# Optimization experiments

Measured on AMD Instinct MI355X. Metric: run time of the kernel, lower is better.

The kernel has to match this reference:

```python
import jax, jax.numpy as jnp
import numpy as np

B, S, H, NH = 2, 2048, 1024, 16
D = H // NH

def setup_inputs() -> dict:
    key = jax.random.key(0)
    ks = jax.random.split(key, 9)
    s = 1.0 / np.sqrt(H)
    return {
        "x": jax.random.normal(ks[0], (B, S, H), jnp.float32),
        "wq": jax.random.uniform(ks[1], (H, H), jnp.float32, -s, s),
        "bq": jax.random.uniform(ks[2], (H,), jnp.float32, -s, s),
        "wk": jax.random.uniform(ks[3], (H, H), jnp.float32, -s, s),
        "bk": jax.random.uniform(ks[4], (H,), jnp.float32, -s, s),
        "wv": jax.random.uniform(ks[5], (H, H), jnp.float32, -s, s),
        "bv": jax.random.uniform(ks[6], (H,), jnp.float32, -s, s),
        "wo": jax.random.uniform(ks[7], (H, H), jnp.float32, -s, s),
        "bo": jax.random.uniform(ks[8], (H,), jnp.float32, -s, s),
    }

def _split_heads(t):
    # [B, S, H] -> [B, NH, S, D]
    return t.reshape(B, S, NH, D).transpose(0, 2, 1, 3)

def reference(x, wq, bq, wk, bk, wv, bv, wo, bo):
    q = _split_heads(x @ wq.T + bq)
    k = _split_heads(x @ wk.T + bk)
    v = _split_heads(x @ wv.T + bv)
    scores = jnp.einsum('bhqd,bhkd->bhqk', q, k) / jnp.sqrt(jnp.float32(D))
    attn = jax.nn.softmax(scores, axis=-1)  # full [B,NH,S,S] materialized as in source
    ctx = jnp.einsum('bhqk,bhkd->bhqd', attn, v)
    concat = ctx.transpose(0, 2, 1, 3).reshape(B, S, H)
    return concat @ wo.T + bo
```

## Files before the change

kernel.cpp:

```cpp
#include <hip/hip_runtime.h>
#include <cstdint>

typedef unsigned short u16;
typedef __attribute__((ext_vector_type(8))) short short8;
typedef __attribute__((ext_vector_type(4))) float f32x4;

#if __has_builtin(__builtin_amdgcn_exp2f)
#define EXP2F(x) __builtin_amdgcn_exp2f(x)
#else
#define EXP2F(x) exp2f(x)
#endif

__device__ inline u16 f2bf(float f) {
  union { float f; unsigned u; } v; v.f = f;
  unsigned u = v.u;
  return (u16)((u + 0x7fffu + ((u >> 16) & 1u)) >> 16);
}

__device__ inline unsigned pk2bf_fast(float a, float b) {
  union { float f; unsigned u; } ua, ub; ua.f = a; ub.f = b;
  return __builtin_amdgcn_perm(ub.u + 0x8000u, ua.u + 0x8000u, 0x07060302u);
}

__device__ inline void gl2lds16(const void* g, void* l) {
  __builtin_amdgcn_global_load_lds(
      (const __attribute__((address_space(1))) unsigned int*)(unsigned long long)(uintptr_t)g,
      (__attribute__((address_space(3))) unsigned int*)(unsigned int)(uintptr_t)l,
      16, 0, 0);
}


__global__ __launch_bounds__(256) void cvt_kernel(
    const float* __restrict__ x,
    const float* __restrict__ wq, const float* __restrict__ wk,
    const float* __restrict__ wv, const float* __restrict__ wo,
    u16* __restrict__ xb, u16* __restrict__ wqb, u16* __restrict__ wkb,
    u16* __restrict__ wvb, u16* __restrict__ wob) {
  const int y = blockIdx.y;
  const int Q = 1 << 20;
  const float* src;
  u16* dst;
  if (y < 4)       { src = x + y * Q; dst = xb + y * Q; }
  else if (y == 4) { src = wq; dst = wqb; }
  else if (y == 5) { src = wk; dst = wkb; }
  else if (y == 6) { src = wv; dst = wvb; }
  else             { src = wo; dst = wob; }
  const int i = (blockIdx.x * 256 + threadIdx.x) * 8;
  float4 a = *(const float4*)(src + i);
  float4 b = *(const float4*)(src + i + 4);
  short8 o;
  o[0] = (short)f2bf(a.x); o[1] = (short)f2bf(a.y);
  o[2] = (short)f2bf(a.z); o[3] = (short)f2bf(a.w);
  o[4] = (short)f2bf(b.x); o[5] = (short)f2bf(b.y);
  o[6] = (short)f2bf(b.z); o[7] = (short)f2bf(b.w);
  const int j = (i & ~63) | (((((i >> 3) & 7) ^ ((i >> 10) & 7))) << 3);
  *(short8*)(dst + j) = o;
}

__global__ __launch_bounds__(256) void gemm_qkv(
    const u16* __restrict__ xb,
    const u16* __restrict__ wqb, const u16* __restrict__ wkb, const u16* __restrict__ wvb,
    const float* __restrict__ bq, const float* __restrict__ bk, const float* __restrict__ bv,
    u16* __restrict__ qo, u16* __restrict__ ko, u16* __restrict__ vto) {
  const int z = blockIdx.z;
  const u16* W = (z == 0) ? wqb : (z == 1) ? wkb : wvb;
  const float* bias = (z == 0) ? bq : (z == 1) ? bk : bv;

  __shared__ u16 smem[24576];
  u16* As = smem;
  u16* Bs = smem + 16384;
  const int tid = threadIdx.x, lane = tid & 63;
  const int wid = tid >> 6;
  const int l15 = lane & 15, lg = lane >> 4;
  const int m0 = blockIdx.y * 128, n0 = blockIdx.x * 64;
  const int sw = ((l15 & 7) << 3);

  f32x4 acc[2][4] = {};

#pragma unroll
  for (int i = 0; i < 4; ++i) {
    int c = i * 256 + tid;
    gl2lds16(xb + (m0 + (c >> 3)) * 1024 + (c & 7) * 8, As + c * 8);
  }
#pragma unroll
  for (int i = 0; i < 2; ++i) {
    int c = i * 256 + tid;
    gl2lds16(W + (n0 + (c >> 3)) * 1024 + (c & 7) * 8, Bs + c * 8);
  }

  for (int k0 = 0; k0 < 1024; k0 += 64) {
    const int p = (k0 >> 6) & 1;
    __syncthreads();
    if (k0 < 960) {
      u16* An = As + (1 - p) * 8192;
      u16* Bn = Bs + (1 - p) * 4096;
#pragma unroll
      for (int i = 0; i < 4; ++i) {
        int c = i * 256 + tid;
        gl2lds16(xb + (m0 + (c >> 3)) * 1024 + k0 + 64 + (c & 7) * 8, An + c * 8);
      }
#pragma unroll
      for (int i = 0; i < 2; ++i) {
        int c = i * 256 + tid;
        gl2lds16(W + (n0 + (c >> 3)) * 1024 + k0 + 64 + (c & 7) * 8, Bn + c * 8);
      }
    }
    const u16* Ap = As + p * 8192;
    const u16* Bp = Bs + p * 4096;
#pragma unroll
    for (int kk = 0; kk < 2; ++kk) {
      short8 af[2], bf[4];
#pragma unroll
      for (int mb = 0; mb < 2; ++mb)
        af[mb] = *(const short8*)(Ap + (wid * 32 + mb * 16 + l15) * 64 + ((((kk * 4 + lg) << 3)) ^ sw));
#pragma unroll
      for (int nb = 0; nb < 4; ++nb)
        bf[nb] = *(const short8*)(Bp + (nb * 16 + l15) * 64 + ((((kk * 4 + lg) << 3)) ^ sw));
#pragma unroll
      for (int mb = 0; mb < 2; ++mb)
#pragma unroll
        for (int nb = 0; nb < 4; ++nb)
          acc[mb][nb] = __builtin_amdgcn_mfma_f32_16x16x32_bf16(af[mb], bf[nb], acc[mb][nb], 0, 0, 0);
    }
  }

  if (z < 2) {
    u16* out = (z == 0) ? qo : ko;
#pragma unroll
    for (int mb = 0; mb < 2; ++mb)
#pragma unroll
      for (int nb = 0; nb < 4; ++nb)
#pragma unroll
        for (int r = 0; r < 4; ++r) {
          int m = m0 + wid * 32 + mb * 16 + lg * 4 + r;
          int n = n0 + nb * 16 + l15;
          float v = acc[mb][nb][r] + bias[n];
          int b = m >> 11, s = m & 2047, hh = n >> 6, d = n & 63;
          out[((b * 16 + hh) * 2048 + s) * 64 + d] = f2bf(v);
        }
  } else {
    __syncthreads();
    u16* wbuf = smem + (wid >> 1) * 4608;
    const int so = (wid & 1) * 2;
#pragma unroll
    for (int mb = 0; mb < 2; ++mb)
#pragma unroll
      for (int nb = 0; nb < 4; ++nb) {
        int n = n0 + nb * 16 + l15;
        float bn = bias[n];
        int dl = nb * 16 + l15;
#pragma unroll
        for (int r = 0; r < 4; ++r) {
          int sig = (lg * 4 + r) * 4 + so + mb;
          wbuf[dl * 72 + sig] = f2bf(acc[mb][nb][r] + bn);
        }
      }
    __syncthreads();
    int hh = n0 >> 6;
    int bb = m0 >> 11;
    int sbase = m0 & 2047;
#pragma unroll
    for (int i = 0; i < 4; ++i) {
      int idx = i * 256 + tid;
      int p2 = idx >> 9, rem = idx & 511;
      int dl = rem >> 3, c = rem & 7;
      short8 vv = *(const short8*)(smem + p2 * 4608 + dl * 72 + c * 8);
      int cs = c ^ (dl & 7);
      *(short8*)(vto + ((bb * 16 + hh) * 64 + dl) * 2048 + sbase + p2 * 64 + cs * 8) = vv;
    }
  }
}

__global__ __launch_bounds__(256, 2) void attn_kernel(
    const u16* __restrict__ qg, const u16* __restrict__ kg,
    const u16* __restrict__ vtg, u16* __restrict__ ctxg) {
  const int h = blockIdx.x, qt = blockIdx.y, b = blockIdx.z;
  const int bh = b * 16 + h;
  const u16* Qg = qg + (bh * 2048 + qt * 128) * 64;
  const u16* Kg = kg + bh * 2048 * 64;
  const u16* Vg = vtg + bh * 64 * 2048;

  __shared__ u16 SP[128 * 72];
  __shared__ u16 Vs[2][4096];

  const int tid = threadIdx.x, lane = tid & 63, wid = tid >> 6;
  const int l15 = lane & 15, lg = lane >> 4;
  const int row0 = wid * 32;
  const int sw = ((l15 & 7) << 3);

  short8 qf[2][2];
#pragma unroll
  for (int mb = 0; mb < 2; ++mb)
#pragma unroll
    for (int kk = 0; kk < 2; ++kk)
      qf[mb][kk] = *(const short8*)(Qg + (row0 + mb * 16 + l15) * 64 + kk * 32 + lg * 8);

  short8 ones8;
#pragma unroll
  for (int j = 0; j < 8; ++j) ones8[j] = (short)0x3F80;

  const u16* kbase = Kg + l15 * 64 + lg * 8;

  short8 kf[2][4];
#pragma unroll
  for (int kk = 0; kk < 2; ++kk)
#pragma unroll
    for (int nb = 0; nb < 4; ++nb)
      kf[kk][nb] = *(const short8*)(kbase + nb * 1024 + kk * 32);

#pragma unroll
  for (int i = 0; i < 2; ++i) {
    int c = i * 256 + tid;
    gl2lds16(Vg + (c >> 3) * 2048 + (c & 7) * 8, &Vs[0][c * 8]);
  }

  f32x4 acc[2][5] = {};
  const float cexp = 0.18033688011112042f;

  for (int kt = 0; kt < 32; ++kt) {
    const int p = kt & 1;
    __syncthreads();
    if (kt < 31) {
#pragma unroll
      for (int i = 0; i < 2; ++i) {
        int c = i * 256 + tid;
        gl2lds16(Vg + (c >> 3) * 2048 + (kt + 1) * 64 + (c & 7) * 8, &Vs[1 - p][c * 8]);
      }
    }
    const u16* Vts = &Vs[p][0];

    f32x4 sc[2][4] = {};
#pragma unroll
    for (int kk = 0; kk < 2; ++kk)
#pragma unroll
      for (int mb = 0; mb < 2; ++mb)
#pragma unroll
        for (int nb = 0; nb < 4; ++nb)
          sc[mb][nb] = __builtin_amdgcn_mfma_f32_16x16x32_bf16(qf[mb][kk], kf[kk][nb], sc[mb][nb], 0, 0, 0);

#pragma unroll
    for (int mb = 0; mb < 2; ++mb)
#pragma unroll
      for (int r = 0; r < 4; ++r) {
        float p0 = EXP2F(fmaf(sc[mb][0][r], cexp, -4.0f));
        float p1 = EXP2F(fmaf(sc[mb][1][r], cexp, -4.0f));
        float p2 = EXP2F(fmaf(sc[mb][2][r], cexp, -4.0f));
        float p3 = EXP2F(fmaf(sc[mb][3][r], cexp, -4.0f));
        uint2 u;
        u.x = pk2bf_fast(p0, p1);
        u.y = pk2bf_fast(p2, p3);
        *(uint2*)(SP + (row0 + mb * 16 + lg * 4 + r) * 72 + l15 * 4) = u;
      }

    {
      const int ktn = (kt + 1 < 32) ? kt + 1 : 0;
#pragma unroll
      for (int kk = 0; kk < 2; ++kk)
#pragma unroll
        for (int nb = 0; nb < 4; ++nb)
          kf[kk][nb] = *(const short8*)(kbase + ktn * 4096 + nb * 1024 + kk * 32);
    }

#pragma unroll
    for (int kk = 0; kk < 2; ++kk) {
      short8 pa[2], vb[4];
#pragma unroll
      for (int mb = 0; mb < 2; ++mb)
        pa[mb] = *(const short8*)(SP + (row0 + mb * 16 + l15) * 72 + kk * 32 + lg * 8);
#pragma unroll
      for (int nd = 0; nd < 4; ++nd)
        vb[nd] = *(const short8*)(Vts + (nd * 16 + l15) * 64 + ((((kk * 4 + lg) << 3)) ^ sw));
#pragma unroll
      for (int mb = 0; mb < 2; ++mb) {
#pragma unroll
        for (int nd = 0; nd < 4; ++nd)
          acc[mb][nd] = __builtin_amdgcn_mfma_f32_16x16x32_bf16(pa[mb], vb[nd], acc[mb][nd], 0, 0, 0);
        acc[mb][4] = __builtin_amdgcn_mfma_f32_16x16x32_bf16(pa[mb], ones8, acc[mb][4], 0, 0, 0);
      }
    }
  }

#pragma unroll
  for (int mb = 0; mb < 2; ++mb)
#pragma unroll
    for (int r = 0; r < 4; ++r) {
      float inv = 1.0f / acc[mb][4][r];
      int s = qt * 128 + row0 + mb * 16 + lg * 4 + r;
      int s7 = s & 7;
      u16* dst = ctxg + (b * 2048 + s) * 1024 + h * 64;
#pragma unroll
      for (int nd = 0; nd < 4; ++nd) {
        int d = nd * 16 + l15;
        int dcol = (((d >> 3) ^ s7) << 3) | (d & 7);
        dst[dcol] = f2bf(acc[mb][nd][r] * inv);
      }
    }
}

__global__ __launch_bounds__(256) void gemm_out(
    const u16* __restrict__ cb, const u16* __restrict__ wob,
    const float* __restrict__ bo, float* __restrict__ out) {
  __shared__ u16 smem[16384];
  u16* As = smem;
  u16* Bs = smem + 8192;
  const int tid = threadIdx.x, lane = tid & 63;
  const int wid = tid >> 6;
  const int l15 = lane & 15, lg = lane >> 4;
  const int m0 = blockIdx.y * 64, n0 = blockIdx.x * 64;
  const int sw = ((l15 & 7) << 3);

  f32x4 acc[4] = {};

#pragma unroll
  for (int i = 0; i < 2; ++i) {
    int c = i * 256 + tid;
    gl2lds16(cb  + (m0 + (c >> 3)) * 1024 + (c & 7) * 8, As + c * 8);
    gl2lds16(wob + (n0 + (c >> 3)) * 1024 + (c & 7) * 8, Bs + c * 8);
  }

  for (int k0 = 0; k0 < 1024; k0 += 64) {
    const int p = (k0 >> 6) & 1;
    __syncthreads();
    if (k0 < 960) {
      u16* An = As + (1 - p) * 4096;
      u16* Bn = Bs + (1 - p) * 4096;
#pragma unroll
      for (int i = 0; i < 2; ++i) {
        int c = i * 256 + tid;
        gl2lds16(cb  + (m0 + (c >> 3)) * 1024 + k0 + 64 + (c & 7) * 8, An + c * 8);
        gl2lds16(wob + (n0 + (c >> 3)) * 1024 + k0 + 64 + (c & 7) * 8, Bn + c * 8);
      }
    }
    const u16* Ap = As + p * 4096;
    const u16* Bp = Bs + p * 4096;
#pragma unroll
    for (int kk = 0; kk < 2; ++kk) {
      short8 af, bf[4];
      af = *(const short8*)(Ap + (wid * 16 + l15) * 64 + ((((kk * 4 + lg) << 3)) ^ sw));
#pragma unroll
      for (int nb = 0; nb < 4; ++nb)
        bf[nb] = *(const short8*)(Bp + (nb * 16 + l15) * 64 + ((((kk * 4 + lg) << 3)) ^ sw));
#pragma unroll
      for (int nb = 0; nb < 4; ++nb)
        acc[nb] = __builtin_amdgcn_mfma_f32_16x16x32_bf16(af, bf[nb], acc[nb], 0, 0, 0);
    }
  }

#pragma unroll
  for (int nb = 0; nb < 4; ++nb)
#pragma unroll
    for (int r = 0; r < 4; ++r) {
      int m = m0 + wid * 16 + lg * 4 + r;
      int n = n0 + nb * 16 + l15;
      out[m * 1024 + n] = acc[nb][r] + bo[n];
    }
}

extern "C" void kernel_launch(void* const* d_in, const int* in_sizes, int n_in,
                              void* d_out, int out_size, void* d_ws, size_t ws_size,
                              hipStream_t stream) {
  const float* x  = (const float*)d_in[0];
  const float* wq = (const float*)d_in[1];
  const float* bq = (const float*)d_in[2];
  const float* wk = (const float*)d_in[3];
  const float* bk = (const float*)d_in[4];
  const float* wv = (const float*)d_in[5];
  const float* bv = (const float*)d_in[6];
  const float* wo = (const float*)d_in[7];
  const float* bo = (const float*)d_in[8];

  if (ws_size < (size_t)24 * 1024 * 1024 * 2) return;
  u16* xb   = (u16*)d_ws;
  u16* wqb  = xb  + (4u << 20);
  u16* wkb  = wqb + (1u << 20);
  u16* wvb  = wkb + (1u << 20);
  u16* wob  = wvb + (1u << 20);
  u16* qb   = wob + (1u << 20);
  u16* kb   = qb  + (4u << 20);
  u16* vtb  = kb  + (4u << 20);
  u16* ctxb = vtb + (4u << 20);

  cvt_kernel<<<dim3(512, 8, 1), 256, 0, stream>>>(x, wq, wk, wv, wo, xb, wqb, wkb, wvb, wob);
  gemm_qkv<<<dim3(16, 32, 3), 256, 0, stream>>>(xb, wqb, wkb, wvb, bq, bk, bv, qb, kb, vtb);
  attn_kernel<<<dim3(16, 16, 2), 256, 0, stream>>>(qb, kb, vtb, ctxb);
  gemm_out<<<dim3(16, 64, 1), 256, 0, stream>>>(ctxb, wob, bo, (float*)d_out);
}
```

Measured before the change: 202.7 us.

## Fuse Q/K/V projections per block, prescale Q, stage K through LDS

The QKV GEMM now computes Q, K and V in one block, so each x tile loaded into LDS is reused by three weight tiles instead of being reloaded across three grid z-slices. The grid shrinks to a third, and LDS and accumulator registers per block grow. The softmax scale is folded into Q at store time, and the constant exp offset is dropped. K is written with an XOR-swizzled column layout. In attention, K is double-buffered through LDS with async copies alongside V, replacing the per-lane global register prefetch. The trade-offs are fewer blocks with higher register and LDS pressure, and a small risk of exp range issues without the offset.

```diff
diff --git a/kernel.cpp b/kernel.cpp
--- a/kernel.cpp
+++ b/kernel.cpp
@@ -57,16 +57,12 @@
   *(short8*)(dst + j) = o;
 }
 
-__global__ __launch_bounds__(256) void gemm_qkv(
+__global__ __launch_bounds__(256, 2) void gemm_qkv(
     const u16* __restrict__ xb,
     const u16* __restrict__ wqb, const u16* __restrict__ wkb, const u16* __restrict__ wvb,
     const float* __restrict__ bq, const float* __restrict__ bk, const float* __restrict__ bv,
     u16* __restrict__ qo, u16* __restrict__ ko, u16* __restrict__ vto) {
-  const int z = blockIdx.z;
-  const u16* W = (z == 0) ? wqb : (z == 1) ? wkb : wvb;
-  const float* bias = (z == 0) ? bq : (z == 1) ? bk : bv;
-
-  __shared__ u16 smem[24576];
+  __shared__ u16 smem[40960];
   u16* As = smem;
   u16* Bs = smem + 16384;
   const int tid = threadIdx.x, lane = tid & 63;
@@ -74,8 +70,9 @@
   const int l15 = lane & 15, lg = lane >> 4;
   const int m0 = blockIdx.y * 128, n0 = blockIdx.x * 64;
   const int sw = ((l15 & 7) << 3);
-
-  f32x4 acc[2][4] = {};
+  const u16* Wz[3] = {wqb, wkb, wvb};
+
+  f32x4 acc[3][2][4] = {};
 
 #pragma unroll
   for (int i = 0; i < 4; ++i) {
@@ -83,63 +80,86 @@
     gl2lds16(xb + (m0 + (c >> 3)) * 1024 + (c & 7) * 8, As + c * 8);
   }
 #pragma unroll
-  for (int i = 0; i < 2; ++i) {
-    int c = i * 256 + tid;
-    gl2lds16(W + (n0 + (c >> 3)) * 1024 + (c & 7) * 8, Bs + c * 8);
-  }
+  for (int z = 0; z < 3; ++z)
+#pragma unroll
+    for (int i = 0; i < 2; ++i) {
+      int c = i * 256 + tid;
+      gl2lds16(Wz[z] + (n0 + (c >> 3)) * 1024 + (c & 7) * 8, Bs + z * 4096 + c * 8);
+    }
 
   for (int k0 = 0; k0 < 1024; k0 += 64) {
     const int p = (k0 >> 6) & 1;
     __syncthreads();
     if (k0 < 960) {
       u16* An = As + (1 - p) * 8192;
-      u16* Bn = Bs + (1 - p) * 4096;
+      u16* Bn = Bs + (1 - p) * 12288;
 #pragma unroll
       for (int i = 0; i < 4; ++i) {
         int c = i * 256 + tid;
         gl2lds16(xb + (m0 + (c >> 3)) * 1024 + k0 + 64 + (c & 7) * 8, An + c * 8);
       }
 #pragma unroll
-      for (int i = 0; i < 2; ++i) {
-        int c = i * 256 + tid;
-        gl2lds16(W + (n0 + (c >> 3)) * 1024 + k0 + 64 + (c & 7) * 8, Bn + c * 8);
-      }
+      for (int z = 0; z < 3; ++z)
+#pragma unroll
+        for (int i = 0; i < 2; ++i) {
+          int c = i * 256 + tid;
+          gl2lds16(Wz[z] + (n0 + (c >> 3)) * 1024 + k0 + 64 + (c & 7) * 8, Bn + z * 4096 + c * 8);
+        }
     }
     const u16* Ap = As + p * 8192;
-    const u16* Bp = Bs + p * 4096;
+    const u16* Bp = Bs + p * 12288;
 #pragma unroll
     for (int kk = 0; kk < 2; ++kk) {
-      short8 af[2], bf[4];
+      short8 af[2], bf[3][4];
 #pragma unroll
       for (int mb = 0; mb < 2; ++mb)
         af[mb] = *(const short8*)(Ap + (wid * 32 + mb * 16 + l15) * 64 + ((((kk * 4 + lg) << 3)) ^ sw));
 #pragma unroll
-      for (int nb = 0; nb < 4; ++nb)
-        bf[nb] = *(const short8*)(Bp + (nb * 16 + l15) * 64 + ((((kk * 4 + lg) << 3)) ^ sw));
-#pragma unroll
-      for (int mb = 0; mb < 2; ++mb)
+      for (int z = 0; z < 3; ++z)
 #pragma unroll
         for (int nb = 0; nb < 4; ++nb)
-          acc[mb][nb] = __builtin_amdgcn_mfma_f32_16x16x32_bf16(af[mb], bf[nb], acc[mb][nb], 0, 0, 0);
-    }
-  }
-
-  if (z < 2) {
-    u16* out = (z == 0) ? qo : ko;
-#pragma unroll
-    for (int mb = 0; mb < 2; ++mb)
-#pragma unroll
-      for (int nb = 0; nb < 4; ++nb)
-#pragma unroll
-        for (int r = 0; r < 4; ++r) {
-          int m = m0 + wid * 32 + mb * 16 + lg * 4 + r;
-          int n = n0 + nb * 16 + l15;
-          float v = acc[mb][nb][r] + bias[n];
-          int b = m >> 11, s = m & 2047, hh = n >> 6, d = n & 63;
-          out[((b * 16 + hh) * 2048 + s) * 64 + d] = f2bf(v);
-        }
-  } else {
-    __syncthreads();
+          bf[z][nb] = *(const short8*)(Bp + z * 4096 + (nb * 16 + l15) * 64 + ((((kk * 4 + lg) << 3)) ^ sw));
+#pragma unroll
+      for (int z = 0; z < 3; ++z)
+#pragma unroll
+        for (int mb = 0; mb < 2; ++mb)
+#pragma unroll
+          for (int nb = 0; nb < 4; ++nb)
+            acc[z][mb][nb] = __builtin_amdgcn_mfma_f32_16x16x32_bf16(af[mb], bf[z][nb], acc[z][mb][nb], 0, 0, 0);
+    }
+  }
+
+  const float cexp = 0.18033688011112042f;
+
+#pragma unroll
+  for (int mb = 0; mb < 2; ++mb)
+#pragma unroll
+    for (int nb = 0; nb < 4; ++nb)
+#pragma unroll
+      for (int r = 0; r < 4; ++r) {
+        int m = m0 + wid * 32 + mb * 16 + lg * 4 + r;
+        int n = n0 + nb * 16 + l15;
+        float v = (acc[0][mb][nb][r] + bq[n]) * cexp;
+        int b = m >> 11, s = m & 2047, hh = n >> 6, d = n & 63;
+        qo[((b * 16 + hh) * 2048 + s) * 64 + d] = f2bf(v);
+      }
+
+#pragma unroll
+  for (int mb = 0; mb < 2; ++mb)
+#pragma unroll
+    for (int nb = 0; nb < 4; ++nb)
+#pragma unroll
+      for (int r = 0; r < 4; ++r) {
+        int m = m0 + wid * 32 + mb * 16 + lg * 4 + r;
+        int n = n0 + nb * 16 + l15;
+        float v = acc[1][mb][nb][r] + bk[n];
+        int b = m >> 11, s = m & 2047, hh = n >> 6, d = n & 63;
+        int dcol = (((d >> 3) ^ (s & 7)) << 3) | (d & 7);
+        ko[((b * 16 + hh) * 2048 + s) * 64 + dcol] = f2bf(v);
+      }
+
+  __syncthreads();
+  {
     u16* wbuf = smem + (wid >> 1) * 4608;
     const int so = (wid & 1) * 2;
 #pragma unroll
@@ -147,12 +167,12 @@
 #pragma unroll
       for (int nb = 0; nb < 4; ++nb) {
         int n = n0 + nb * 16 + l15;
-        float bn = bias[n];
+        float bn = bv[n];
         int dl = nb * 16 + l15;
 #pragma unroll
         for (int r = 0; r < 4; ++r) {
           int sig = (lg * 4 + r) * 4 + so + mb;
-          wbuf[dl * 72 + sig] = f2bf(acc[mb][nb][r] + bn);
+          wbuf[dl * 72 + sig] = f2bf(acc[2][mb][nb][r] + bn);
         }
       }
     __syncthreads();
@@ -181,7 +201,7 @@
   const u16* Vg = vtg + bh * 64 * 2048;
 
   __shared__ u16 SP[128 * 72];
-  __shared__ u16 Vs[2][4096];
+  __shared__ u16 KV[2][8192];
 
   const int tid = threadIdx.x, lane = tid & 63, wid = tid >> 6;
   const int l15 = lane & 15, lg = lane >> 4;
@@ -199,23 +219,14 @@
 #pragma unroll
   for (int j = 0; j < 8; ++j) ones8[j] = (short)0x3F80;
 
-  const u16* kbase = Kg + l15 * 64 + lg * 8;
-
-  short8 kf[2][4];
-#pragma unroll
-  for (int kk = 0; kk < 2; ++kk)
-#pragma unroll
-    for (int nb = 0; nb < 4; ++nb)
-      kf[kk][nb] = *(const short8*)(kbase + nb * 1024 + kk * 32);
-
 #pragma unroll
   for (int i = 0; i < 2; ++i) {
     int c = i * 256 + tid;
-    gl2lds16(Vg + (c >> 3) * 2048 + (c & 7) * 8, &Vs[0][c * 8]);
+    gl2lds16(Kg + c * 8, &KV[0][c * 8]);
+    gl2lds16(Vg + (c >> 3) * 2048 + (c & 7) * 8, &KV[0][4096 + c * 8]);
   }
 
   f32x4 acc[2][5] = {};
-  const float cexp = 0.18033688011112042f;
 
   for (int kt = 0; kt < 32; ++kt) {
     const int p = kt & 1;
@@ -224,42 +235,40 @@
 #pragma unroll
       for (int i = 0; i < 2; ++i) {
         int c = i * 256 + tid;
-        gl2lds16(Vg + (c >> 3) * 2048 + (kt + 1) * 64 + (c & 7) * 8, &Vs[1 - p][c * 8]);
-      }
-    }
-    const u16* Vts = &Vs[p][0];
+        gl2lds16(Kg + (kt + 1) * 4096 + c * 8, &KV[1 - p][c * 8]);
+        gl2lds16(Vg + (c >> 3) * 2048 + (kt + 1) * 64 + (c & 7) * 8, &KV[1 - p][4096 + c * 8]);
+      }
+    }
+    const u16* Ks = &KV[p][0];
+    const u16* Vts = &KV[p][4096];
 
     f32x4 sc[2][4] = {};
 #pragma unroll
-    for (int kk = 0; kk < 2; ++kk)
+    for (int kk = 0; kk < 2; ++kk) {
+      short8 bfr[4];
+#pragma unroll
+      for (int nb = 0; nb < 4; ++nb)
+        bfr[nb] = *(const short8*)(Ks + (nb * 16 + l15) * 64 + ((((kk * 4 + lg) << 3)) ^ sw));
 #pragma unroll
       for (int mb = 0; mb < 2; ++mb)
 #pragma unroll
         for (int nb = 0; nb < 4; ++nb)
-          sc[mb][nb] = __builtin_amdgcn_mfma_f32_16x16x32_bf16(qf[mb][kk], kf[kk][nb], sc[mb][nb], 0, 0, 0);
+          sc[mb][nb] = __builtin_amdgcn_mfma_f32_16x16x32_bf16(qf[mb][kk], bfr[nb], sc[mb][nb], 0, 0, 0);
+    }
 
 #pragma unroll
     for (int mb = 0; mb < 2; ++mb)
 #pragma unroll
       for (int r = 0; r < 4; ++r) {
-        float p0 = EXP2F(fmaf(sc[mb][0][r], cexp, -4.0f));
-        float p1 = EXP2F(fmaf(sc[mb][1][r], cexp, -4.0f));
-        float p2 = EXP2F(fmaf(sc[mb][2][r], cexp, -4.0f));
-        float p3 = EXP2F(fmaf(sc[mb][3][r], cexp, -4.0f));
+        float p0 = EXP2F(sc[mb][0][r]);
+        float p1 = EXP2F(sc[mb][1][r]);
+        float p2 = EXP2F(sc[mb][2][r]);
+        float p3 = EXP2F(sc[mb][3][r]);
         uint2 u;
         u.x = pk2bf_fast(p0, p1);
         u.y = pk2bf_fast(p2, p3);
         *(uint2*)(SP + (row0 + mb * 16 + lg * 4 + r) * 72 + l15 * 4) = u;
       }
-
-    {
-      const int ktn = (kt + 1 < 32) ? kt + 1 : 0;
-#pragma unroll
-      for (int kk = 0; kk < 2; ++kk)
-#pragma unroll
-        for (int nb = 0; nb < 4; ++nb)
-          kf[kk][nb] = *(const short8*)(kbase + ktn * 4096 + nb * 1024 + kk * 32);
-    }
 
 #pragma unroll
     for (int kk = 0; kk < 2; ++kk) {
@@ -381,7 +390,7 @@
   u16* ctxb = vtb + (4u << 20);
 
   cvt_kernel<<<dim3(512, 8, 1), 256, 0, stream>>>(x, wq, wk, wv, wo, xb, wqb, wkb, wvb, wob);
-  gemm_qkv<<<dim3(16, 32, 3), 256, 0, stream>>>(xb, wqb, wkb, wvb, bq, bk, bv, qb, kb, vtb);
+  gemm_qkv<<<dim3(16, 32, 1), 256, 0, stream>>>(xb, wqb, wkb, wvb, bq, bk, bv, qb, kb, vtb);
   attn_kernel<<<dim3(16, 16, 2), 256, 0, stream>>>(qb, kb, vtb, ctxb);
   gemm_out<<<dim3(16, 64, 1), 256, 0, stream>>>(ctxb, wob, bo, (float*)d_out);
 }
```

New measurement: 180.3 us. 1.12x faster.
